# Performance work log

Measured on AMD Instinct MI355X. Metric: run time of the kernel, lower is better.

## Reference

```python
import jax, jax.numpy as jnp
import numpy as np

B, N, D, E = 1024, 64, 128, 512   # pairs, nodes/graph, input_dim, edges/graph
G = 128                           # gcn hidden size (all 3 layers)
C1, C2, K = 8, 16, 5              # conv channels, kernel size


def setup_inputs() -> dict:
    key = jax.random.key(0)
    ks = jax.random.split(key, 12)
    NT = B * N
    x_q = jax.random.normal(ks[0], (NT, D), jnp.float32)
    x_c = jax.random.normal(ks[1], (NT, D), jnp.float32)
    offs = jnp.repeat(jnp.arange(B, dtype=jnp.int32) * N, E)

    def edges(k):
        k1, k2 = jax.random.split(k)
        src = jax.random.randint(k1, (B * E,), 0, N, jnp.int32) + offs
        dst = jax.random.randint(k2, (B * E,), 0, N, jnp.int32) + offs
        return jnp.stack([src, dst])

    edge_index_q = edges(ks[2])
    edge_index_c = edges(ks[3])

    def lin(k, fi, fo):
        return jax.random.normal(k, (fi, fo), jnp.float32) / np.sqrt(fi)

    gcn_w0 = lin(ks[4], D, G); gcn_b0 = jnp.zeros((G,), jnp.float32)
    gcn_w1 = lin(ks[5], G, G); gcn_b1 = jnp.zeros((G,), jnp.float32)
    gcn_w2 = lin(ks[6], G, G); gcn_b2 = jnp.zeros((G,), jnp.float32)
    conv1_w = jax.random.normal(ks[7], (3, C1, 1, K, K), jnp.float32) / np.sqrt(K * K)
    conv1_b = jnp.zeros((3, C1), jnp.float32)
    conv2_w = jax.random.normal(ks[8], (3, C2, C1, K, K), jnp.float32) / np.sqrt(C1 * K * K)
    conv2_b = jnp.zeros((3, C2), jnp.float32)
    F = 3 * C2 * (N // 4) * (N // 4)  # 12288 = linear_size[0]
    lin_w = lin(ks[9], F, 512); lin_b = jnp.zeros((512,), jnp.float32)
    score_w = lin(ks[10], 512, 1); score_b = jnp.zeros((1,), jnp.float32)
    return dict(x_q=x_q, x_c=x_c, gcn_w0=gcn_w0, gcn_b0=gcn_b0, gcn_w1=gcn_w1,
                gcn_b1=gcn_b1, gcn_w2=gcn_w2, gcn_b2=gcn_b2, conv1_w=conv1_w,
                conv1_b=conv1_b, conv2_w=conv2_w, conv2_b=conv2_b, lin_w=lin_w,
                lin_b=lin_b, score_w=score_w, score_b=score_b,
                edge_index_q=edge_index_q, edge_index_c=edge_index_c)


def _gcn_pass(x, ei, params):
    # pyg GCNConv: add self loops, symmetric D^-1/2 norm, scatter-add, +bias.
    n = x.shape[0]
    loops = jnp.arange(n, dtype=ei.dtype)
    s = jnp.concatenate([ei[0], loops])
    d = jnp.concatenate([ei[1], loops])
    deg = jax.ops.segment_sum(jnp.ones(s.shape[0], x.dtype), d, num_segments=n)
    dis = jax.lax.rsqrt(deg)  # deg >= 1 due to self loops
    norm = (dis[s] * dis[d])[:, None]
    feats, h = [], x
    for w, b in params:
        m = h @ w
        out = jax.ops.segment_sum(m[s] * norm, d, num_segments=n) + b
        feats.append(out)        # pre-relu features, as in GCN_pass
        h = jax.nn.relu(out)
    return feats


def _conv(x, w, b):
    # ZeroPad2d(2) + Conv2d(k=5, stride=1): spatial-size preserving
    y = jax.lax.conv_general_dilated(x, w, (1, 1), [(2, 2), (2, 2)],
                                     dimension_numbers=('NCHW', 'OIHW', 'NCHW'))
    return y + b[None, :, None, None]


def _maxpool2(x):
    # ZeroPad2d((0,1,0,1)) + MaxPool2d(k=2, s=2)
    xp = jnp.pad(x, ((0, 0), (0, 0), (0, 1), (0, 1)))
    return jax.lax.reduce_window(xp, -jnp.inf, jax.lax.max,
                                 (1, 1, 2, 2), (1, 1, 2, 2), 'VALID')


def reference(x_q, x_c, gcn_w0, gcn_b0, gcn_w1, gcn_b1, gcn_w2, gcn_b2,
              conv1_w, conv1_b, conv2_w, conv2_b, lin_w, lin_b,
              score_w, score_b, edge_index_q, edge_index_c):
    params = [(gcn_w0, gcn_b0), (gcn_w1, gcn_b1), (gcn_w2, gcn_b2)]
    fq = _gcn_pass(x_q, edge_index_q, params)
    fc = _gcn_pass(x_c, edge_index_c, params)
    # all graphs have exactly N nodes -> pad_sequence/pad_matrix are reshapes
    sims = jnp.stack([jnp.einsum('bnd,bmd->bnm', q.reshape(B, N, -1),
                                 c.reshape(B, N, -1)) for q, c in zip(fq, fc)])
    f = sims[:, :, None]                                  # [3, B, 1, N, N]
    f = jax.vmap(_maxpool2)(jax.nn.relu(jax.vmap(_conv)(f, conv1_w, conv1_b)))
    f = jax.vmap(_maxpool2)(jax.nn.relu(jax.vmap(_conv)(f, conv2_w, conv2_b)))
    # torch.cat along channel dim, then view(-1, 12288)
    feat = jnp.concatenate([f[0], f[1], f[2]], axis=1).reshape(B, -1)
    h = jax.nn.relu(feat @ lin_w + lin_b)
    return (h @ score_w + score_b).reshape(-1)
```

## Files before the change

kernel.cpp:

```cpp
#include <hip/hip_runtime.h>

constexpr int NB = 1024;
constexpr int NN = 64;
constexpr int ND = 128;
constexpr int NE = 512;
constexpr int FEAT_F = 12288;

typedef __attribute__((ext_vector_type(8))) short short8v;
typedef __attribute__((ext_vector_type(4))) float f32x4;
typedef __fp16 h2v __attribute__((ext_vector_type(2)));

__device__ inline ushort f2bf(float x) {
    unsigned u = __float_as_uint(x);
    u += 0x7FFFu + ((u >> 16) & 1u);
    return (ushort)(u >> 16);
}

__global__ __launch_bounds__(256)
void adj_kernel(const int* __restrict__ esq, const int* __restrict__ edq,
                const int* __restrict__ esc, const int* __restrict__ edc,
                ushort* __restrict__ Aq, ushort* __restrict__ Ac)
{
    __shared__ float A[NN * NN];
    __shared__ float dis[NN];
    const int b = blockIdx.x, side = blockIdx.y, tid = threadIdx.x;
    const int* es = side ? esc : esq;
    const int* ed = side ? edc : edq;
    ushort* Aout = side ? Ac : Aq;

    for (int i = tid; i < NN * NN; i += 256) A[i] = 0.f;
    __syncthreads();
    for (int e = tid; e < NE; e += 256) {
        const int s = es[b * NE + e] & (NN - 1);
        const int d = ed[b * NE + e] & (NN - 1);
        atomicAdd(&A[d * NN + s], 1.0f);
    }
    __syncthreads();
    if (tid < NN) {
        float sum = 1.0f;
        for (int s = 0; s < NN; s++) sum += A[tid * NN + s];
        dis[tid] = rsqrtf(sum);
    }
    __syncthreads();
    for (int i = tid; i < NN * NN; i += 256) {
        const int d = i >> 6, s = i & 63;
        float v = A[i];
        if (d == s) v += 1.0f;
        Aout[(size_t)b * (NN * NN) + i] = f2bf(dis[d] * v * dis[s]);
    }
}

__global__ __launch_bounds__(256)
void castw_kernel(const float* __restrict__ w0, const float* __restrict__ w1,
                  const float* __restrict__ w2, ushort* __restrict__ wtb)
{
    const float* W = blockIdx.x == 0 ? w0 : (blockIdx.x == 1 ? w1 : w2);
    ushort* out = wtb + (size_t)blockIdx.x * ND * ND;
    for (int i = threadIdx.x; i < ND * ND; i += 256) {
        const int f = i >> 7, k = i & 127;
        out[i] = f2bf(W[k * ND + f]);
    }
}

__global__ __launch_bounds__(256)
void gcn_mfma_kernel(const void* __restrict__ hq_in, const void* __restrict__ hc_in,
                     const ushort* __restrict__ Aqb, const ushort* __restrict__ Acb,
                     const ushort* __restrict__ wt_l, const float* __restrict__ bias,
                     ushort* __restrict__ outq, ushort* __restrict__ outc, int first)
{
    __shared__ ushort ht[64][132];
    __shared__ ushort wt[128][132];
    __shared__ ushort mT[128][68];
    __shared__ ushort as_[64][68];

    const int b = blockIdx.x, side = blockIdx.y, tid = threadIdx.x;
    const int lane = tid & 63, w = tid >> 6;
    const int q = lane >> 4, rf = lane & 15;

    const ushort* Ab = (side ? Acb : Aqb) + (size_t)b * 4096;
    ushort* outp = (side ? outc : outq) + (size_t)b * 8192;

    {
        const int sr = tid >> 2, sc = (tid & 3) * 32;
        if (first) {
            const float* hin = (const float*)(side ? hc_in : hq_in) + (size_t)b * 8192 + sr * 128 + sc;
            #pragma unroll
            for (int j = 0; j < 4; j++) {
                const float4 v0 = *(const float4*)&hin[8 * j];
                const float4 v1 = *(const float4*)&hin[8 * j + 4];
                *(ushort4*)&ht[sr][sc + 8 * j]     = make_ushort4(f2bf(v0.x), f2bf(v0.y), f2bf(v0.z), f2bf(v0.w));
                *(ushort4*)&ht[sr][sc + 8 * j + 4] = make_ushort4(f2bf(v1.x), f2bf(v1.y), f2bf(v1.z), f2bf(v1.w));
            }
        } else {
            const ushort* hin = (const ushort*)(side ? hc_in : hq_in) + (size_t)b * 8192 + sr * 128 + sc;
            #pragma unroll
            for (int j = 0; j < 4; j++) {
                short8v v = *(const short8v*)&hin[8 * j];
                #pragma unroll
                for (int e = 0; e < 8; e++) {
                    const ushort u = (ushort)v[e];
                    v[e] = (short)((u & 0x8000u) ? 0u : u);
                }
                *(short8v*)&ht[sr][sc + 8 * j] = v;
            }
        }
    }
    {
        const int wr = tid >> 1, wc = (tid & 1) * 64;
        const ushort* src = wt_l + wr * 128 + wc;
        #pragma unroll
        for (int j = 0; j < 8; j++)
            *(short8v*)&wt[wr][wc + 8 * j] = *(const short8v*)&src[8 * j];
    }
    {
        const int ar = tid >> 2, ac = (tid & 3) * 16;
        const ushort* src = Ab + ar * 64 + ac;
        *(short8v*)&as_[ar][ac]     = *(const short8v*)&src[0];
        *(short8v*)&as_[ar][ac + 8] = *(const short8v*)&src[8];
    }
    __syncthreads();

    {
        f32x4 acc1[8];
        #pragma unroll
        for (int cb = 0; cb < 8; cb++) acc1[cb] = f32x4{0.f, 0.f, 0.f, 0.f};
        short8v af[4];
        #pragma unroll
        for (int ks = 0; ks < 4; ks++)
            af[ks] = *(const short8v*)&ht[16 * w + rf][32 * ks + 8 * q];
        #pragma unroll
        for (int cb = 0; cb < 8; cb++)
            #pragma unroll
            for (int ks = 0; ks < 4; ks++) {
                const short8v bf = *(const short8v*)&wt[16 * cb + rf][32 * ks + 8 * q];
                acc1[cb] = __builtin_amdgcn_mfma_f32_16x16x32_bf16(af[ks], bf, acc1[cb], 0, 0, 0);
            }
        #pragma unroll
        for (int cb = 0; cb < 8; cb++)
            *(ushort4*)&mT[16 * cb + rf][16 * w + 4 * q] =
                make_ushort4(f2bf(acc1[cb][0]), f2bf(acc1[cb][1]), f2bf(acc1[cb][2]), f2bf(acc1[cb][3]));
    }
    __syncthreads();

    {
        f32x4 acc2[8];
        #pragma unroll
        for (int cb = 0; cb < 8; cb++) acc2[cb] = f32x4{0.f, 0.f, 0.f, 0.f};
        short8v af2[2];
        #pragma unroll
        for (int ks = 0; ks < 2; ks++)
            af2[ks] = *(const short8v*)&as_[16 * w + rf][32 * ks + 8 * q];
        #pragma unroll
        for (int cb = 0; cb < 8; cb++)
            #pragma unroll
            for (int ks = 0; ks < 2; ks++) {
                const short8v bf2 = *(const short8v*)&mT[16 * cb + rf][32 * ks + 8 * q];
                acc2[cb] = __builtin_amdgcn_mfma_f32_16x16x32_bf16(af2[ks], bf2, acc2[cb], 0, 0, 0);
            }
        #pragma unroll
        for (int cb = 0; cb < 8; cb++) {
            const float bb = bias[16 * cb + rf];
            #pragma unroll
            for (int r = 0; r < 4; r++)
                outp[(16 * w + 4 * q + r) * 128 + 16 * cb + rf] = f2bf(acc2[cb][r] + bb);
        }
    }
}

__global__ __launch_bounds__(256)
void sims_mfma_kernel(const ushort* __restrict__ hq0, const ushort* __restrict__ hc0,
                      const ushort* __restrict__ hq1, const ushort* __restrict__ hc1,
                      const ushort* __restrict__ hq2, const ushort* __restrict__ hc2,
                      float* __restrict__ S)
{
    __shared__ ushort q_s[64][132];
    __shared__ ushort c_s[64][132];
    const int b = blockIdx.x, l = blockIdx.y, tid = threadIdx.x;
    const int lane = tid & 63, w = tid >> 6;
    const int q = lane >> 4, rf = lane & 15;
    const ushort* hq = (l == 0 ? hq0 : (l == 1 ? hq1 : hq2)) + (size_t)b * 8192;
    const ushort* hc = (l == 0 ? hc0 : (l == 1 ? hc1 : hc2)) + (size_t)b * 8192;

    {
        const int sr = tid >> 2, sc = (tid & 3) * 32;
        #pragma unroll
        for (int j = 0; j < 4; j++) {
            *(short8v*)&q_s[sr][sc + 8 * j] = *(const short8v*)&hq[sr * 128 + sc + 8 * j];
            *(short8v*)&c_s[sr][sc + 8 * j] = *(const short8v*)&hc[sr * 128 + sc + 8 * j];
        }
    }
    __syncthreads();

    f32x4 acc[4];
    #pragma unroll
    for (int cb = 0; cb < 4; cb++) acc[cb] = f32x4{0.f, 0.f, 0.f, 0.f};
    short8v af[4];
    #pragma unroll
    for (int ks = 0; ks < 4; ks++)
        af[ks] = *(const short8v*)&q_s[16 * w + rf][32 * ks + 8 * q];
    #pragma unroll
    for (int cb = 0; cb < 4; cb++)
        #pragma unroll
        for (int ks = 0; ks < 4; ks++) {
            const short8v bf = *(const short8v*)&c_s[16 * cb + rf][32 * ks + 8 * q];
            acc[cb] = __builtin_amdgcn_mfma_f32_16x16x32_bf16(af[ks], bf, acc[cb], 0, 0, 0);
        }
    float* out = S + ((size_t)l * NB + b) * 4096;
    #pragma unroll
    for (int cb = 0; cb < 4; cb++)
        #pragma unroll
        for (int r = 0; r < 4; r++)
            out[(16 * w + 4 * q + r) * 64 + 16 * cb + rf] = acc[cb][r];
}

__global__ __launch_bounds__(256)
void conv_kernel(const float* __restrict__ simsb,
                 const float* __restrict__ c1w, const float* __restrict__ c1b,
                 const float* __restrict__ c2w, const float* __restrict__ c2b,
                 ushort* __restrict__ featb)
{
    __shared__ float img[68 * 68];
    __shared__ ushort p1b[36 * 36 * 8];
    __shared__ ushort w2s[16][232];

    const int b = blockIdx.x, l = blockIdx.y, tid = threadIdx.x;
    const int lane = tid & 63, wid = tid >> 6;
    const int q = lane >> 4, rf = lane & 15;

    for (int i = tid; i < 68 * 68; i += 256) img[i] = 0.f;
    for (int i = tid; i < 36 * 36 * 8 / 2; i += 256) ((uint*)p1b)[i] = 0u;
    for (int i = tid; i < 16 * 224; i += 256) {
        const int co = i / 224, k = i - co * 224;
        const int tap = k >> 3, ci = k & 7;
        w2s[co][k] = (tap < 25) ? f2bf(c2w[l * 3200 + co * 200 + ci * 25 + tap])
                                : (ushort)0;
    }
    __syncthreads();
    for (int i = tid; i < 4096; i += 256) {
        const int y = i >> 6, x = i & 63;
        img[(y + 2) * 68 + (x + 2)] = simsb[((size_t)l * NB + b) * 4096 + i];
    }
    __syncthreads();

    {
        const int by = tid >> 4, bx = tid & 15;
        float mv[2][2][8];
#if __has_builtin(__builtin_amdgcn_fdot2)
        h2v pe[8][4], po[8][4];
        #pragma unroll
        for (int r = 0; r < 8; r++) {
            float x[8];
            #pragma unroll
            for (int c2 = 0; c2 < 4; c2++) {
                const float2 v = *(const float2*)&img[(4 * by + r) * 68 + 4 * bx + 2 * c2];
                x[2 * c2] = v.x; x[2 * c2 + 1] = v.y;
            }
            #pragma unroll
            for (int m = 0; m < 4; m++) {
                pe[r][m] = __builtin_amdgcn_cvt_pkrtz(x[2 * m], x[2 * m + 1]);
                po[r][m] = __builtin_amdgcn_cvt_pkrtz(x[2 * m + 1], (m < 3) ? x[2 * m + 2] : x[7]);
            }
        }
        for (int c = 0; c < 8; c++) {
            h2v wp[5][3];
            #pragma unroll
            for (int ky = 0; ky < 5; ky++) {
                const float w0 = c1w[l * 200 + c * 25 + 5 * ky];
                const float w1 = c1w[l * 200 + c * 25 + 5 * ky + 1];
                const float w2 = c1w[l * 200 + c * 25 + 5 * ky + 2];
                const float w3 = c1w[l * 200 + c * 25 + 5 * ky + 3];
                const float w4 = c1w[l * 200 + c * 25 + 5 * ky + 4];
                wp[ky][0] = __builtin_amdgcn_cvt_pkrtz(w0, w1);
                wp[ky][1] = __builtin_amdgcn_cvt_pkrtz(w2, w3);
                wp[ky][2] = __builtin_amdgcn_cvt_pkrtz(w4, 0.f);
            }
            const float bb = c1b[l * 8 + c];
            #pragma unroll
            for (int jy = 0; jy < 2; jy++)
                #pragma unroll
                for (int jx = 0; jx < 2; jx++) {
                    float mm = 0.f;
                    #pragma unroll
                    for (int dy = 0; dy < 2; dy++)
                        #pragma unroll
                        for (int dx = 0; dx < 2; dx++) {
                            const int Y = 2 * jy + dy, X = 2 * jx + dx, m0 = X >> 1;
                            float a = bb;
                            #pragma unroll
                            for (int ky = 0; ky < 5; ky++) {
                                if (X & 1) {
                                    a = __builtin_amdgcn_fdot2(po[Y + ky][m0],     wp[ky][0], a, false);
                                    a = __builtin_amdgcn_fdot2(po[Y + ky][m0 + 1], wp[ky][1], a, false);
                                    a = __builtin_amdgcn_fdot2(po[Y + ky][m0 + 2], wp[ky][2], a, false);
                                } else {
                                    a = __builtin_amdgcn_fdot2(pe[Y + ky][m0],     wp[ky][0], a, false);
                                    a = __builtin_amdgcn_fdot2(pe[Y + ky][m0 + 1], wp[ky][1], a, false);
                                    a = __builtin_amdgcn_fdot2(pe[Y + ky][m0 + 2], wp[ky][2], a, false);
                                }
                            }
                            mm = fmaxf(mm, a);
                        }
                    mv[jy][jx][c] = mm;
                }
        }
#else
        float pt[8][8];
        #pragma unroll
        for (int r = 0; r < 8; r++)
            #pragma unroll
            for (int c2 = 0; c2 < 4; c2++) {
                const float2 v = *(const float2*)&img[(4 * by + r) * 68 + 4 * bx + 2 * c2];
                pt[r][2 * c2] = v.x; pt[r][2 * c2 + 1] = v.y;
            }
        for (int c = 0; c < 8; c++) {
            float wr[25];
            #pragma unroll
            for (int t = 0; t < 25; t++) wr[t] = c1w[l * 200 + c * 25 + t];
            const float bb = c1b[l * 8 + c];
            #pragma unroll
            for (int jy = 0; jy < 2; jy++)
                #pragma unroll
                for (int jx = 0; jx < 2; jx++) {
                    float mm = 0.f;
                    #pragma unroll
                    for (int dy = 0; dy < 2; dy++)
                        #pragma unroll
                        for (int dx = 0; dx < 2; dx++) {
                            float a = bb;
                            #pragma unroll
                            for (int ky = 0; ky < 5; ky++)
                                #pragma unroll
                                for (int kx = 0; kx < 5; kx++)
                                    a += pt[2 * jy + dy + ky][2 * jx + dx + kx] * wr[ky * 5 + kx];
                            mm = fmaxf(mm, a);
                        }
                    mv[jy][jx][c] = mm;
                }
        }
#endif
        #pragma unroll
        for (int jy = 0; jy < 2; jy++)
            #pragma unroll
            for (int jx = 0; jx < 2; jx++) {
                const int pos = (2 * by + jy + 2) * 36 + (2 * bx + jx + 2);
                *(ushort4*)&p1b[pos * 8] =
                    make_ushort4(f2bf(mv[jy][jx][0]), f2bf(mv[jy][jx][1]),
                                 f2bf(mv[jy][jx][2]), f2bf(mv[jy][jx][3]));
                *(ushort4*)&p1b[pos * 8 + 4] =
                    make_ushort4(f2bf(mv[jy][jx][4]), f2bf(mv[jy][jx][5]),
                                 f2bf(mv[jy][jx][6]), f2bf(mv[jy][jx][7]));
            }
    }
    __syncthreads();

    short8v bf[7];
    #pragma unroll
    for (int ks = 0; ks < 7; ks++)
        bf[ks] = *(const short8v*)&w2s[rf][32 * ks + 8 * q];
    const float bb2 = c2b[l * 16 + rf];

    for (int t = 0; t < 4; t++) {
        const int r = wid + 4 * t;
        f32x4 acc00 = {0.f,0.f,0.f,0.f}, acc01 = acc00, acc10 = acc00, acc11 = acc00;
        #pragma unroll
        for (int ks = 0; ks < 7; ks++) {
            const int tap = 4 * ks + q;
            const int dy = tap / 5, dx = tap - 5 * dy;
            const bool dum = tap >= 25;
            const int row0 = dum ? 35 : (2 * r + dy);
            const int row1 = dum ? 35 : (2 * r + 1 + dy);
            const int cb   = (dum ? 0 : dx) + rf;
            const short8v a00 = *(const short8v*)&p1b[(row0 * 36 + cb) * 8];
            const short8v a01 = *(const short8v*)&p1b[(row0 * 36 + cb + 16) * 8];
            const short8v a10 = *(const short8v*)&p1b[(row1 * 36 + cb) * 8];
            const short8v a11 = *(const short8v*)&p1b[(row1 * 36 + cb + 16) * 8];
            acc00 = __builtin_amdgcn_mfma_f32_16x16x32_bf16(a00, bf[ks], acc00, 0, 0, 0);
            acc01 = __builtin_amdgcn_mfma_f32_16x16x32_bf16(a01, bf[ks], acc01, 0, 0, 0);
            acc10 = __builtin_amdgcn_mfma_f32_16x16x32_bf16(a10, bf[ks], acc10, 0, 0, 0);
            acc11 = __builtin_amdgcn_mfma_f32_16x16x32_bf16(a11, bf[ks], acc11, 0, 0, 0);
        }
        const float v0 = fmaxf(fmaxf(fmaxf(acc00[0], acc00[1]), fmaxf(acc10[0], acc10[1])) + bb2, 0.f);
        const float v1 = fmaxf(fmaxf(fmaxf(acc00[2], acc00[3]), fmaxf(acc10[2], acc10[3])) + bb2, 0.f);
        const float v2 = fmaxf(fmaxf(fmaxf(acc01[0], acc01[1]), fmaxf(acc11[0], acc11[1])) + bb2, 0.f);
        const float v3 = fmaxf(fmaxf(fmaxf(acc01[2], acc01[3]), fmaxf(acc11[2], acc11[3])) + bb2, 0.f);
        const size_t base = (size_t)b * FEAT_F + ((size_t)l * 16 + rf) * 256 + r * 16;
        featb[base + 2 * q]         = f2bf(v0);
        featb[base + 2 * q + 1]     = f2bf(v1);
        featb[base + 8 + 2 * q]     = f2bf(v2);
        featb[base + 8 + 2 * q + 1] = f2bf(v3);
    }
}

__global__ __launch_bounds__(256)
void cast_lwT_kernel(const float* __restrict__ lw, ushort* __restrict__ lwT)
{
    __shared__ ushort t[32][34];
    const int kb = blockIdx.x * 32, nb2 = blockIdx.y * 32;
    const int x = threadIdx.x & 31, y = threadIdx.x >> 5;
    #pragma unroll
    for (int j = 0; j < 4; j++) {
        const int yy = y + 8 * j;
        t[x][yy] = f2bf(lw[(size_t)(kb + yy) * 512 + nb2 + x]);
    }
    __syncthreads();
    #pragma unroll
    for (int j = 0; j < 4; j++) {
        const int yy = y + 8 * j;
        lwT[(size_t)(nb2 + yy) * FEAT_F + kb + x] = t[yy][x];
    }
}

__global__ __launch_bounds__(256)
void lin_mfma_kernel(const ushort* __restrict__ featb, const ushort* __restrict__ lwT,
                     float* __restrict__ hacc8)
{
    __shared__ ushort a_s[64][40];
    __shared__ ushort b_s[64][40];
    const int nb = blockIdx.x, mb = blockIdx.y, kz = blockIdx.z;
    const int tid = threadIdx.x;
    const int wid = tid >> 6, lane = tid & 63;
    const int wm = wid >> 1, wn = wid & 1;
    const int m0 = mb * 64, n0 = nb * 64;
    const size_t k0 = (size_t)kz * 1536;

    const int sr = tid >> 2;
    const int sk = (tid & 3) * 8;
    const int kf = (lane >> 4) * 8;
    const int rf = lane & 15;

    f32x4 zero = {0.f, 0.f, 0.f, 0.f};
    f32x4 acc00 = zero, acc01 = zero, acc10 = zero, acc11 = zero;

    for (int ks = 0; ks < 48; ks++) {
        const size_t kc = k0 + (size_t)ks * 32;
        *(short8v*)&a_s[sr][sk] = *(const short8v*)&featb[(size_t)(m0 + sr) * FEAT_F + kc + sk];
        *(short8v*)&b_s[sr][sk] = *(const short8v*)&lwT[(size_t)(n0 + sr) * FEAT_F + kc + sk];
        __syncthreads();
        short8v af0 = *(const short8v*)&a_s[wm * 32 + rf][kf];
        short8v af1 = *(const short8v*)&a_s[wm * 32 + 16 + rf][kf];
        short8v bf0 = *(const short8v*)&b_s[wn * 32 + rf][kf];
        short8v bf1 = *(const short8v*)&b_s[wn * 32 + 16 + rf][kf];
        acc00 = __builtin_amdgcn_mfma_f32_16x16x32_bf16(af0, bf0, acc00, 0, 0, 0);
        acc01 = __builtin_amdgcn_mfma_f32_16x16x32_bf16(af0, bf1, acc01, 0, 0, 0);
        acc10 = __builtin_amdgcn_mfma_f32_16x16x32_bf16(af1, bf0, acc10, 0, 0, 0);
        acc11 = __builtin_amdgcn_mfma_f32_16x16x32_bf16(af1, bf1, acc11, 0, 0, 0);
        __syncthreads();
    }
    float* outz = hacc8 + (size_t)kz * 1024 * 512;
    const int rbase = m0 + wm * 32 + (lane >> 4) * 4;
    const int cbase = n0 + wn * 32 + rf;
    #pragma unroll
    for (int r = 0; r < 4; r++) {
        outz[(size_t)(rbase + r) * 512 + cbase]           = acc00[r];
        outz[(size_t)(rbase + r) * 512 + cbase + 16]      = acc01[r];
        outz[(size_t)(rbase + 16 + r) * 512 + cbase]      = acc10[r];
        outz[(size_t)(rbase + 16 + r) * 512 + cbase + 16] = acc11[r];
    }
}

__global__ __launch_bounds__(256)
void score_kernel(const float* __restrict__ hacc8, const float* __restrict__ lb,
                  const float* __restrict__ sw, const float* __restrict__ sb,
                  float* __restrict__ outp)
{
    const int b = blockIdx.x, tid = threadIdx.x;
    float v = 0.f;
    for (int j = tid; j < 512; j += 256) {
        float s = lb[j];
        #pragma unroll
        for (int z = 0; z < 8; z++)
            s += hacc8[((size_t)z * 1024 + b) * 512 + j];
        v += fmaxf(s, 0.f) * sw[j];
    }
    #pragma unroll
    for (int off = 32; off > 0; off >>= 1) v += __shfl_down(v, off);
    __shared__ float red[4];
    if ((tid & 63) == 0) red[tid >> 6] = v;
    __syncthreads();
    if (tid == 0) outp[b] = red[0] + red[1] + red[2] + red[3] + sb[0];
}

extern "C" void kernel_launch(void* const* d_in, const int* in_sizes, int n_in,
                              void* d_out, int out_size, void* d_ws, size_t ws_size,
                              hipStream_t stream)
{
    const float* x_q = (const float*)d_in[0];
    const float* x_c = (const float*)d_in[1];
    const float* gw[3] = {(const float*)d_in[2], (const float*)d_in[4], (const float*)d_in[6]};
    const float* gb[3] = {(const float*)d_in[3], (const float*)d_in[5], (const float*)d_in[7]};
    const float* c1w = (const float*)d_in[8];
    const float* c1b = (const float*)d_in[9];
    const float* c2w = (const float*)d_in[10];
    const float* c2b = (const float*)d_in[11];
    const float* lw  = (const float*)d_in[12];
    const float* lb  = (const float*)d_in[13];
    const float* sw  = (const float*)d_in[14];
    const float* sb  = (const float*)d_in[15];
    const int* eq = (const int*)d_in[16];
    const int* ec = (const int*)d_in[17];

    char* p = (char*)d_ws;
    ushort* hq0 = (ushort*)p; p += (size_t)NB * 8192 * 2;
    ushort* hc0 = (ushort*)p; p += (size_t)NB * 8192 * 2;
    ushort* hq1 = (ushort*)p; p += (size_t)NB * 8192 * 2;
    ushort* hc1 = (ushort*)p; p += (size_t)NB * 8192 * 2;
    ushort* hq2 = (ushort*)p; p += (size_t)NB * 8192 * 2;
    ushort* hc2 = (ushort*)p; p += (size_t)NB * 8192 * 2;
    ushort* Aqb = (ushort*)p; p += (size_t)NB * 4096 * 2;
    ushort* Acb = (ushort*)p; p += (size_t)NB * 4096 * 2;
    ushort* wtb = (ushort*)p; p += (size_t)3 * ND * ND * 2;
    float* simsb = (float*)p; p += (size_t)3 * NB * 4096 * 4;
    float* hacc8 = (float*)p; p += (size_t)8 * NB * 512 * 4;
    ushort* featb = (ushort*)p; p += (size_t)NB * FEAT_F * 2;
    ushort* lwT   = (ushort*)p; p += (size_t)512 * FEAT_F * 2;
    float* outf = (float*)d_out;

    const int* esq = eq;
    const int* edq = eq + (size_t)NB * NE;
    const int* esc = ec;
    const int* edc = ec + (size_t)NB * NE;

    adj_kernel<<<dim3(NB, 2), 256, 0, stream>>>(esq, edq, esc, edc, Aqb, Acb);
    castw_kernel<<<3, 256, 0, stream>>>(gw[0], gw[1], gw[2], wtb);
    cast_lwT_kernel<<<dim3(FEAT_F / 32, 512 / 32), 256, 0, stream>>>(lw, lwT);

    gcn_mfma_kernel<<<dim3(NB, 2), 256, 0, stream>>>(x_q, x_c, Aqb, Acb, wtb,
                                                     gb[0], hq0, hc0, 1);
    gcn_mfma_kernel<<<dim3(NB, 2), 256, 0, stream>>>(hq0, hc0, Aqb, Acb, wtb + ND * ND,
                                                     gb[1], hq1, hc1, 0);
    gcn_mfma_kernel<<<dim3(NB, 2), 256, 0, stream>>>(hq1, hc1, Aqb, Acb, wtb + 2 * ND * ND,
                                                     gb[2], hq2, hc2, 0);

    sims_mfma_kernel<<<dim3(NB, 3), 256, 0, stream>>>(hq0, hc0, hq1, hc1, hq2, hc2, simsb);

    conv_kernel<<<dim3(NB, 3), 256, 0, stream>>>(simsb, c1w, c1b, c2w, c2b, featb);

    lin_mfma_kernel<<<dim3(8, 16, 8), 256, 0, stream>>>(featb, lwT, hacc8);
    score_kernel<<<NB, 256, 0, stream>>>(hacc8, lb, sw, sb, outf);
}
```

Before: 404.7 us.

## Fuse similarity GEMM into conv kernel and drop LDS staging in GCN

The separate sims kernel is removed. The conv kernel now computes the 64x64 similarity matrix with MFMA directly from the bf16 node features and writes it into its padded LDS image, so the fp32 sims buffer no longer makes a round trip through global memory. The GCN kernel also stops staging H, W and A in shared memory: MFMA fragments are loaded straight from global memory, which removes the staging copies, one barrier and most of the LDS footprint. The cost is uncoalesced, repeated global reads of the weight fragments by every block, which relies on cache hits instead of LDS reuse.

```diff
diff --git a/kernel.cpp b/kernel.cpp
--- a/kernel.cpp
+++ b/kernel.cpp
@@ -68,10 +68,7 @@
                      const ushort* __restrict__ wt_l, const float* __restrict__ bias,
                      ushort* __restrict__ outq, ushort* __restrict__ outc, int first)
 {
-    __shared__ ushort ht[64][132];
-    __shared__ ushort wt[128][132];
     __shared__ ushort mT[128][68];
-    __shared__ ushort as_[64][68];
 
     const int b = blockIdx.x, side = blockIdx.y, tid = threadIdx.x;
     const int lane = tid & 63, w = tid >> 6;
@@ -80,59 +77,45 @@
     const ushort* Ab = (side ? Acb : Aqb) + (size_t)b * 4096;
     ushort* outp = (side ? outc : outq) + (size_t)b * 8192;
 
-    {
-        const int sr = tid >> 2, sc = (tid & 3) * 32;
-        if (first) {
-            const float* hin = (const float*)(side ? hc_in : hq_in) + (size_t)b * 8192 + sr * 128 + sc;
-            #pragma unroll
-            for (int j = 0; j < 4; j++) {
-                const float4 v0 = *(const float4*)&hin[8 * j];
-                const float4 v1 = *(const float4*)&hin[8 * j + 4];
-                *(ushort4*)&ht[sr][sc + 8 * j]     = make_ushort4(f2bf(v0.x), f2bf(v0.y), f2bf(v0.z), f2bf(v0.w));
-                *(ushort4*)&ht[sr][sc + 8 * j + 4] = make_ushort4(f2bf(v1.x), f2bf(v1.y), f2bf(v1.z), f2bf(v1.w));
-            }
-        } else {
-            const ushort* hin = (const ushort*)(side ? hc_in : hq_in) + (size_t)b * 8192 + sr * 128 + sc;
-            #pragma unroll
-            for (int j = 0; j < 4; j++) {
-                short8v v = *(const short8v*)&hin[8 * j];
-                #pragma unroll
-                for (int e = 0; e < 8; e++) {
-                    const ushort u = (ushort)v[e];
-                    v[e] = (short)((u & 0x8000u) ? 0u : u);
-                }
-                *(short8v*)&ht[sr][sc + 8 * j] = v;
-            }
-        }
-    }
-    {
-        const int wr = tid >> 1, wc = (tid & 1) * 64;
-        const ushort* src = wt_l + wr * 128 + wc;
-        #pragma unroll
-        for (int j = 0; j < 8; j++)
-            *(short8v*)&wt[wr][wc + 8 * j] = *(const short8v*)&src[8 * j];
-    }
-    {
-        const int ar = tid >> 2, ac = (tid & 3) * 16;
-        const ushort* src = Ab + ar * 64 + ac;
-        *(short8v*)&as_[ar][ac]     = *(const short8v*)&src[0];
-        *(short8v*)&as_[ar][ac + 8] = *(const short8v*)&src[8];
-    }
-    __syncthreads();
+    short8v af[4];
+    if (first) {
+        const float* hin = (const float*)(side ? hc_in : hq_in)
+                         + (size_t)b * 8192 + (16 * w + rf) * 128;
+        #pragma unroll
+        for (int ks = 0; ks < 4; ks++) {
+            const float4 v0 = *(const float4*)&hin[32 * ks + 8 * q];
+            const float4 v1 = *(const float4*)&hin[32 * ks + 8 * q + 4];
+            short8v v;
+            v[0] = (short)f2bf(v0.x); v[1] = (short)f2bf(v0.y);
+            v[2] = (short)f2bf(v0.z); v[3] = (short)f2bf(v0.w);
+            v[4] = (short)f2bf(v1.x); v[5] = (short)f2bf(v1.y);
+            v[6] = (short)f2bf(v1.z); v[7] = (short)f2bf(v1.w);
+            af[ks] = v;
+        }
+    } else {
+        const ushort* hin = (const ushort*)(side ? hc_in : hq_in)
+                          + (size_t)b * 8192 + (16 * w + rf) * 128;
+        #pragma unroll
+        for (int ks = 0; ks < 4; ks++) {
+            short8v v = *(const short8v*)&hin[32 * ks + 8 * q];
+            #pragma unroll
+            for (int e = 0; e < 8; e++) {
+                const ushort u = (ushort)v[e];
+                v[e] = (short)((u & 0x8000u) ? 0u : u);
+            }
+            af[ks] = v;
+        }
+    }
 
     {
         f32x4 acc1[8];
         #pragma unroll
         for (int cb = 0; cb < 8; cb++) acc1[cb] = f32x4{0.f, 0.f, 0.f, 0.f};
-        short8v af[4];
-        #pragma unroll
-        for (int ks = 0; ks < 4; ks++)
-            af[ks] = *(const short8v*)&ht[16 * w + rf][32 * ks + 8 * q];
         #pragma unroll
         for (int cb = 0; cb < 8; cb++)
             #pragma unroll
             for (int ks = 0; ks < 4; ks++) {
-                const short8v bf = *(const short8v*)&wt[16 * cb + rf][32 * ks + 8 * q];
+                const short8v bf = *(const short8v*)&wt_l[(size_t)(16 * cb + rf) * 128 + 32 * ks + 8 * q];
                 acc1[cb] = __builtin_amdgcn_mfma_f32_16x16x32_bf16(af[ks], bf, acc1[cb], 0, 0, 0);
             }
         #pragma unroll
@@ -143,13 +126,13 @@
     __syncthreads();
 
     {
+        short8v af2[2];
+        #pragma unroll
+        for (int ks = 0; ks < 2; ks++)
+            af2[ks] = *(const short8v*)&Ab[(size_t)(16 * w + rf) * 64 + 32 * ks + 8 * q];
         f32x4 acc2[8];
         #pragma unroll
         for (int cb = 0; cb < 8; cb++) acc2[cb] = f32x4{0.f, 0.f, 0.f, 0.f};
-        short8v af2[2];
-        #pragma unroll
-        for (int ks = 0; ks < 2; ks++)
-            af2[ks] = *(const short8v*)&as_[16 * w + rf][32 * ks + 8 * q];
         #pragma unroll
         for (int cb = 0; cb < 8; cb++)
             #pragma unroll
@@ -168,53 +151,9 @@
 }
 
 __global__ __launch_bounds__(256)
-void sims_mfma_kernel(const ushort* __restrict__ hq0, const ushort* __restrict__ hc0,
-                      const ushort* __restrict__ hq1, const ushort* __restrict__ hc1,
-                      const ushort* __restrict__ hq2, const ushort* __restrict__ hc2,
-                      float* __restrict__ S)
-{
-    __shared__ ushort q_s[64][132];
-    __shared__ ushort c_s[64][132];
-    const int b = blockIdx.x, l = blockIdx.y, tid = threadIdx.x;
-    const int lane = tid & 63, w = tid >> 6;
-    const int q = lane >> 4, rf = lane & 15;
-    const ushort* hq = (l == 0 ? hq0 : (l == 1 ? hq1 : hq2)) + (size_t)b * 8192;
-    const ushort* hc = (l == 0 ? hc0 : (l == 1 ? hc1 : hc2)) + (size_t)b * 8192;
-
-    {
-        const int sr = tid >> 2, sc = (tid & 3) * 32;
-        #pragma unroll
-        for (int j = 0; j < 4; j++) {
-            *(short8v*)&q_s[sr][sc + 8 * j] = *(const short8v*)&hq[sr * 128 + sc + 8 * j];
-            *(short8v*)&c_s[sr][sc + 8 * j] = *(const short8v*)&hc[sr * 128 + sc + 8 * j];
-        }
-    }
-    __syncthreads();
-
-    f32x4 acc[4];
-    #pragma unroll
-    for (int cb = 0; cb < 4; cb++) acc[cb] = f32x4{0.f, 0.f, 0.f, 0.f};
-    short8v af[4];
-    #pragma unroll
-    for (int ks = 0; ks < 4; ks++)
-        af[ks] = *(const short8v*)&q_s[16 * w + rf][32 * ks + 8 * q];
-    #pragma unroll
-    for (int cb = 0; cb < 4; cb++)
-        #pragma unroll
-        for (int ks = 0; ks < 4; ks++) {
-            const short8v bf = *(const short8v*)&c_s[16 * cb + rf][32 * ks + 8 * q];
-            acc[cb] = __builtin_amdgcn_mfma_f32_16x16x32_bf16(af[ks], bf, acc[cb], 0, 0, 0);
-        }
-    float* out = S + ((size_t)l * NB + b) * 4096;
-    #pragma unroll
-    for (int cb = 0; cb < 4; cb++)
-        #pragma unroll
-        for (int r = 0; r < 4; r++)
-            out[(16 * w + 4 * q + r) * 64 + 16 * cb + rf] = acc[cb][r];
-}
-
-__global__ __launch_bounds__(256)
-void conv_kernel(const float* __restrict__ simsb,
+void conv_kernel(const ushort* __restrict__ hq0, const ushort* __restrict__ hc0,
+                 const ushort* __restrict__ hq1, const ushort* __restrict__ hc1,
+                 const ushort* __restrict__ hq2, const ushort* __restrict__ hc2,
                  const float* __restrict__ c1w, const float* __restrict__ c1b,
                  const float* __restrict__ c2w, const float* __restrict__ c2b,
                  ushort* __restrict__ featb)
@@ -226,6 +165,9 @@
     const int b = blockIdx.x, l = blockIdx.y, tid = threadIdx.x;
     const int lane = tid & 63, wid = tid >> 6;
     const int q = lane >> 4, rf = lane & 15;
+
+    const ushort* hq = (l == 0 ? hq0 : (l == 1 ? hq1 : hq2)) + (size_t)b * 8192;
+    const ushort* hc = (l == 0 ? hc0 : (l == 1 ? hc1 : hc2)) + (size_t)b * 8192;
 
     for (int i = tid; i < 68 * 68; i += 256) img[i] = 0.f;
     for (int i = tid; i < 36 * 36 * 8 / 2; i += 256) ((uint*)p1b)[i] = 0u;
@@ -236,9 +178,24 @@
                                 : (ushort)0;
     }
     __syncthreads();
-    for (int i = tid; i < 4096; i += 256) {
-        const int y = i >> 6, x = i & 63;
-        img[(y + 2) * 68 + (x + 2)] = simsb[((size_t)l * NB + b) * 4096 + i];
+
+    {
+        short8v afq[4];
+        #pragma unroll
+        for (int ks = 0; ks < 4; ks++)
+            afq[ks] = *(const short8v*)&hq[(size_t)(16 * wid + rf) * 128 + 32 * ks + 8 * q];
+        #pragma unroll
+        for (int cb = 0; cb < 4; cb++) {
+            f32x4 acc = {0.f, 0.f, 0.f, 0.f};
+            #pragma unroll
+            for (int ks = 0; ks < 4; ks++) {
+                const short8v bf = *(const short8v*)&hc[(size_t)(16 * cb + rf) * 128 + 32 * ks + 8 * q];
+                acc = __builtin_amdgcn_mfma_f32_16x16x32_bf16(afq[ks], bf, acc, 0, 0, 0);
+            }
+            #pragma unroll
+            for (int r = 0; r < 4; r++)
+                img[(16 * wid + 4 * q + r + 2) * 68 + (16 * cb + rf + 2)] = acc[r];
+        }
     }
     __syncthreads();
 
@@ -509,7 +466,6 @@
     ushort* Aqb = (ushort*)p; p += (size_t)NB * 4096 * 2;
     ushort* Acb = (ushort*)p; p += (size_t)NB * 4096 * 2;
     ushort* wtb = (ushort*)p; p += (size_t)3 * ND * ND * 2;
-    float* simsb = (float*)p; p += (size_t)3 * NB * 4096 * 4;
     float* hacc8 = (float*)p; p += (size_t)8 * NB * 512 * 4;
     ushort* featb = (ushort*)p; p += (size_t)NB * FEAT_F * 2;
     ushort* lwT   = (ushort*)p; p += (size_t)512 * FEAT_F * 2;
@@ -531,9 +487,8 @@
     gcn_mfma_kernel<<<dim3(NB, 2), 256, 0, stream>>>(hq1, hc1, Aqb, Acb, wtb + 2 * ND * ND,
                                                      gb[2], hq2, hc2, 0);
 
-    sims_mfma_kernel<<<dim3(NB, 3), 256, 0, stream>>>(hq0, hc0, hq1, hc1, hq2, hc2, simsb);
-
-    conv_kernel<<<dim3(NB, 3), 256, 0, stream>>>(simsb, c1w, c1b, c2w, c2b, featb);
+    conv_kernel<<<dim3(NB, 3), 256, 0, stream>>>(hq0, hc0, hq1, hc1, hq2, hc2,
+                                                 c1w, c1b, c2w, c2b, featb);
 
     lin_mfma_kernel<<<dim3(8, 16, 8), 256, 0, stream>>>(featb, lwT, hacc8);
     score_kernel<<<NB, 256, 0, stream>>>(hacc8, lb, sw, sb, outf);
```

After: 438.5 us. +8.3%, slower.
